# Kernel optimization log

Measured on AMD Instinct MI355X. Metric: run time of the kernel, lower is better.

## Reference

```python
import jax, jax.numpy as jnp
import numpy as np

N_SRC0, N_DST0, N_DST1 = 100000, 25000, 5000
E0, E1 = 800000, 160000
D = 256


def setup_inputs() -> dict:
    key = jax.random.key(0)
    k = jax.random.split(key, 7)
    return {
        "x": jax.random.normal(k[0], (N_SRC0, D), dtype=jnp.float32),
        "ew0": jax.random.uniform(k[1], (E0,), dtype=jnp.float32),
        "ew1": jax.random.uniform(k[2], (E1,), dtype=jnp.float32),
        "src0": jax.random.randint(k[3], (E0,), 0, N_SRC0, dtype=jnp.int32),
        "dst0": jax.random.randint(k[4], (E0,), 0, N_DST0, dtype=jnp.int32),
        "src1": jax.random.randint(k[5], (E1,), 0, N_DST0, dtype=jnp.int32),
        "dst1": jax.random.randint(k[6], (E1,), 0, N_DST1, dtype=jnp.int32),
    }


def _block(x, src, dst, ew, n_dst):
    # u_mul_e + sum: gather src features, scale by edge weight, scatter-sum to dst
    msgs = x[src] * ew[:, None]            # [E, D]
    return jax.ops.segment_sum(msgs, dst, num_segments=n_dst)  # [n_dst, D]


def reference(x, ew0, ew1, src0, dst0, src1, dst1):
    h = _block(x, src0, dst0, ew0, N_DST0)   # block 0: [N_DST0, D]
    h = _block(h, src1, dst1, ew1, N_DST1)   # block 1: [N_DST1, D]
    return h
```

## Files before the change

kernel.cpp:

```cpp
#include <hip/hip_runtime.h>

constexpr int D      = 256;
constexpr int DV4    = D / 4;
constexpr int N_DST0 = 25000;
constexpr int N_DST1 = 5000;
constexpr int CAP    = 96;


__device__ __forceinline__ unsigned pack_bf16(float a, float b) {
    unsigned ua = __float_as_uint(a);
    unsigned ub = __float_as_uint(b);
    ua = (ua + 0x7FFFu + ((ua >> 16) & 1u)) >> 16;
    ub = (ub + 0x7FFFu + ((ub >> 16) & 1u)) >> 16;
    return ua | (ub << 16);
}

__device__ __forceinline__ void fma8_bf16(float* acc, uint4 v, float w) {
    acc[0] += __uint_as_float(v.x << 16)          * w;
    acc[1] += __uint_as_float(v.x & 0xFFFF0000u)  * w;
    acc[2] += __uint_as_float(v.y << 16)          * w;
    acc[3] += __uint_as_float(v.y & 0xFFFF0000u)  * w;
    acc[4] += __uint_as_float(v.z << 16)          * w;
    acc[5] += __uint_as_float(v.z & 0xFFFF0000u)  * w;
    acc[6] += __uint_as_float(v.w << 16)          * w;
    acc[7] += __uint_as_float(v.w & 0xFFFF0000u)  * w;
}


__global__ __launch_bounds__(256) void prep_fused(
    const float4* __restrict__ x4, uint2* __restrict__ xb, int n4,
    const int* __restrict__ src0, const float* __restrict__ ew0,
    const int* __restrict__ dst0, int E0, int* __restrict__ cnt0,
    unsigned long long* __restrict__ meta0,
    const int* __restrict__ src1, const float* __restrict__ ew1,
    const int* __restrict__ dst1, int E1, int* __restrict__ cnt1,
    unsigned long long* __restrict__ meta1)
{
    int third = blockIdx.x / 3;
    int role  = blockIdx.x % 3;
    int nGrp  = gridDim.x / 3;

    if (role < 2) {
        int cb = third * 2 + role;
        int i = cb * blockDim.x + threadIdx.x;
        int stride = nGrp * 2 * blockDim.x;
        for (; i < n4; i += stride) {
            float4 v = x4[i];
            xb[i] = make_uint2(pack_bf16(v.x, v.y), pack_bf16(v.z, v.w));
        }
    } else {
        int T = nGrp * blockDim.x;
        int i0 = third * blockDim.x + threadIdx.x;
        int total = E0 + E1;
        for (int base = i0; base < total; base += 4 * T) {
            int  s[4]; float w[4]; int d[4]; int which[4]; bool ok[4];
            #pragma unroll
            for (int j = 0; j < 4; ++j) {
                int i = base + j * T;
                ok[j] = i < total;
                if (ok[j]) {
                    if (i < E0) { s[j]=src0[i]; w[j]=ew0[i]; d[j]=dst0[i]; which[j]=0; }
                    else { int q=i-E0; s[j]=src1[q]; w[j]=ew1[q]; d[j]=dst1[q]; which[j]=1; }
                }
            }
            int p[4];
            #pragma unroll
            for (int j = 0; j < 4; ++j) {
                if (ok[j]) p[j] = atomicAdd(which[j] ? &cnt1[d[j]] : &cnt0[d[j]], 1);
            }
            #pragma unroll
            for (int j = 0; j < 4; ++j) {
                if (ok[j] && p[j] < CAP) {
                    unsigned long long v =
                        (unsigned long long)(unsigned)s[j] |
                        ((unsigned long long)__float_as_uint(w[j]) << 32);
                    unsigned long long* dstp =
                        (which[j] ? meta1 : meta0) + (size_t)d[j] * CAP + p[j];
                    __builtin_nontemporal_store(v, dstp);
                }
            }
        }
    }
}


template <bool OUT_BF16>
__global__ __launch_bounds__(256) void gather_cap(
    const uint4* __restrict__ xb4,
    const int2*  __restrict__ meta,
    const int*   __restrict__ cnt,
    void*        __restrict__ outp,
    int n_dst)
{
    int wave = (int)((blockIdx.x * blockDim.x + threadIdx.x) >> 6);
    int lane = threadIdx.x & 63;
    if (wave >= n_dst) return;

    int half = lane >> 5;
    int c16  = lane & 31;

    int n = min(cnt[wave], CAP);
    const int2* m = meta + (size_t)wave * CAP;

    float acc[8] = {0.f,0.f,0.f,0.f,0.f,0.f,0.f,0.f};

    for (int base = 0; base < n; base += 64) {
        int idx = base + lane;
        int2 mm = (idx < n) ? m[idx] : make_int2(0, 0);
        int nk = min(64, n - base);

        for (int e = 0; e < nk; e += 8) {
            int   sA = __shfl(mm.x, e + 0 + half, 64);
            int   sB = __shfl(mm.x, e + 2 + half, 64);
            int   sC = __shfl(mm.x, e + 4 + half, 64);
            int   sD = __shfl(mm.x, e + 6 + half, 64);
            float wA = __int_as_float(__shfl(mm.y, e + 0 + half, 64));
            float wB = __int_as_float(__shfl(mm.y, e + 2 + half, 64));
            float wC = __int_as_float(__shfl(mm.y, e + 4 + half, 64));
            float wD = __int_as_float(__shfl(mm.y, e + 6 + half, 64));
            uint4 vA = xb4[(size_t)sA * 32 + c16];
            uint4 vB = xb4[(size_t)sB * 32 + c16];
            uint4 vC = xb4[(size_t)sC * 32 + c16];
            uint4 vD = xb4[(size_t)sD * 32 + c16];
            fma8_bf16(acc, vA, wA);
            fma8_bf16(acc, vB, wB);
            fma8_bf16(acc, vC, wC);
            fma8_bf16(acc, vD, wD);
        }
    }

    #pragma unroll
    for (int j = 0; j < 8; ++j) acc[j] += __shfl_xor(acc[j], 32, 64);

    if (half == 0) {
        if (OUT_BF16) {
            uint4 o;
            o.x = pack_bf16(acc[0], acc[1]);
            o.y = pack_bf16(acc[2], acc[3]);
            o.z = pack_bf16(acc[4], acc[5]);
            o.w = pack_bf16(acc[6], acc[7]);
            ((uint4*)outp)[(size_t)wave * 32 + c16] = o;
        } else {
            float4* o4 = (float4*)outp;
            o4[(size_t)wave * 64 + c16 * 2 + 0] = make_float4(acc[0], acc[1], acc[2], acc[3]);
            o4[(size_t)wave * 64 + c16 * 2 + 1] = make_float4(acc[4], acc[5], acc[6], acc[7]);
        }
    }
}


__global__ __launch_bounds__(256) void hist_both(
    const int* __restrict__ dst0, int E0, int* __restrict__ cnt0,
    const int* __restrict__ dst1, int E1, int* __restrict__ cnt1)
{
    int i = blockIdx.x * blockDim.x + threadIdx.x;
    int stride = gridDim.x * blockDim.x;
    int total = E0 + E1;
    for (; i < total; i += stride) {
        if (i < E0) atomicAdd(&cnt0[dst0[i]], 1);
        else        atomicAdd(&cnt1[dst1[i - E0]], 1);
    }
}

__device__ void scan_one(int* cnt, int* row, int n)
{
    const int T = 1024;
    int t   = threadIdx.x;
    int per = (n + T - 1) / T;
    int b   = t * per;
    int e   = min(b + per, n);

    int local = 0;
    for (int i = b; i < e; ++i) local += cnt[i];

    int lane = t & 63, wid = t >> 6;
    int v = local;
    #pragma unroll
    for (int off = 1; off < 64; off <<= 1) {
        int u = __shfl_up(v, off, 64);
        if (lane >= off) v += u;
    }

    __shared__ int wsum[16], woff[16];
    if (lane == 63) wsum[wid] = v;
    __syncthreads();
    if (t == 0) {
        int run = 0;
        #pragma unroll
        for (int i = 0; i < 16; ++i) { woff[i] = run; run += wsum[i]; }
        row[n] = run;
    }
    __syncthreads();

    int run = woff[wid] + (v - local);
    for (int i = b; i < e; ++i) {
        int c = cnt[i];
        row[i] = run;
        cnt[i] = run;
        run += c;
    }
}

__global__ __launch_bounds__(1024) void scan_both(
    int* cnt0, int* row0, int n0, int* cnt1, int* row1, int n1)
{
    if (blockIdx.x == 0) scan_one(cnt0, row0, n0);
    else                 scan_one(cnt1, row1, n1);
}

__global__ __launch_bounds__(256) void scatter_both(
    const int* __restrict__ src0, const float* __restrict__ ew0,
    const int* __restrict__ dst0, int E0, int* __restrict__ cur0,
    int2* __restrict__ meta0,
    const int* __restrict__ src1, const float* __restrict__ ew1,
    const int* __restrict__ dst1, int E1, int* __restrict__ cur1,
    int2* __restrict__ meta1)
{
    int i = blockIdx.x * blockDim.x + threadIdx.x;
    int stride = gridDim.x * blockDim.x;
    int total = E0 + E1;
    for (; i < total; i += stride) {
        if (i < E0) {
            int p = atomicAdd(&cur0[dst0[i]], 1);
            meta0[p] = make_int2(src0[i], __float_as_int(ew0[i]));
        } else {
            int j = i - E0;
            int p = atomicAdd(&cur1[dst1[j]], 1);
            meta1[p] = make_int2(src1[j], __float_as_int(ew1[j]));
        }
    }
}

__global__ __launch_bounds__(256) void gather_rows_f32(
    const float* __restrict__ xin,
    const int2*  __restrict__ meta,
    const int*   __restrict__ row_start,
    float*       __restrict__ outp,
    int n_dst)
{
    int wave = (int)((blockIdx.x * blockDim.x + threadIdx.x) >> 6);
    int lane = threadIdx.x & 63;
    if (wave >= n_dst) return;

    int beg = row_start[wave];
    int end = row_start[wave + 1];
    const float4* xv = reinterpret_cast<const float4*>(xin);

    float4 acc = {0.f, 0.f, 0.f, 0.f};
    for (int base = beg; base < end; base += 64) {
        int idx = base + lane;
        int2 m = (idx < end) ? meta[idx] : make_int2(0, 0);
        int nk = min(64, end - base);
        int k = 0;
        for (; k + 4 <= nk; k += 4) {
            float4 v0 = xv[(size_t)__shfl(m.x, k + 0, 64) * DV4 + lane];
            float4 v1 = xv[(size_t)__shfl(m.x, k + 1, 64) * DV4 + lane];
            float4 v2 = xv[(size_t)__shfl(m.x, k + 2, 64) * DV4 + lane];
            float4 v3 = xv[(size_t)__shfl(m.x, k + 3, 64) * DV4 + lane];
            float w0 = __int_as_float(__shfl(m.y, k + 0, 64));
            float w1 = __int_as_float(__shfl(m.y, k + 1, 64));
            float w2 = __int_as_float(__shfl(m.y, k + 2, 64));
            float w3 = __int_as_float(__shfl(m.y, k + 3, 64));
            acc.x += v0.x * w0; acc.y += v0.y * w0; acc.z += v0.z * w0; acc.w += v0.w * w0;
            acc.x += v1.x * w1; acc.y += v1.y * w1; acc.z += v1.z * w1; acc.w += v1.w * w1;
            acc.x += v2.x * w2; acc.y += v2.y * w2; acc.z += v2.z * w2; acc.w += v2.w * w2;
            acc.x += v3.x * w3; acc.y += v3.y * w3; acc.z += v3.z * w3; acc.w += v3.w * w3;
        }
        for (; k < nk; ++k) {
            float4 v = xv[(size_t)__shfl(m.x, k, 64) * DV4 + lane];
            float w  = __int_as_float(__shfl(m.y, k, 64));
            acc.x += v.x * w; acc.y += v.y * w; acc.z += v.z * w; acc.w += v.w * w;
        }
    }
    reinterpret_cast<float4*>(outp)[(size_t)wave * DV4 + lane] = acc;
}


extern "C" void kernel_launch(void* const* d_in, const int* in_sizes, int n_in,
                              void* d_out, int out_size, void* d_ws, size_t ws_size,
                              hipStream_t stream) {
    const float* x    = (const float*)d_in[0];
    const float* ew0  = (const float*)d_in[1];
    const float* ew1  = (const float*)d_in[2];
    const int*   src0 = (const int*)d_in[3];
    const int*   dst0 = (const int*)d_in[4];
    const int*   src1 = (const int*)d_in[5];
    const int*   dst1 = (const int*)d_in[6];
    float*       out  = (float*)d_out;

    const int E0    = in_sizes[1];
    const int E1    = in_sizes[2];
    const int N_SRC = in_sizes[0] / D;

    const int blk = 256;
    int g0 = (N_DST0 * 64 + blk - 1) / blk;
    int g1 = (N_DST1 * 64 + blk - 1) / blk;
    int n4 = N_SRC * D / 4;

    size_t need_t1 =
        (size_t)N_SRC * D * 2 +
        (size_t)N_DST0 * D * 2 +
        (size_t)N_DST0 * CAP * 8 +
        (size_t)N_DST1 * CAP * 8 +
        (size_t)(N_DST0 + N_DST1) * 4 + 1024;

    if (ws_size >= need_t1) {
        char* p = (char*)d_ws;
        uint2* xb    = (uint2*)p; p += (size_t)N_SRC * D * 2;
        uint2* h0b   = (uint2*)p; p += (size_t)N_DST0 * D * 2;
        unsigned long long* meta0 = (unsigned long long*)p; p += (size_t)N_DST0 * CAP * 8;
        unsigned long long* meta1 = (unsigned long long*)p; p += (size_t)N_DST1 * CAP * 8;
        int*   cnt0  = (int*)p;   p += (size_t)N_DST0 * 4;
        int*   cnt1  = (int*)p;   p += (size_t)N_DST1 * 4;

        hipMemsetAsync(cnt0, 0, (size_t)(N_DST0 + N_DST1) * 4, stream);

        const int grid = 3072;
        prep_fused<<<grid, blk, 0, stream>>>(
            (const float4*)x, xb, n4,
            src0, ew0, dst0, E0, cnt0, meta0,
            src1, ew1, dst1, E1, cnt1, meta1);

        gather_cap<true ><<<g0, blk, 0, stream>>>(
            (const uint4*)xb,  (const int2*)meta0, cnt0, (void*)h0b, N_DST0);
        gather_cap<false><<<g1, blk, 0, stream>>>(
            (const uint4*)h0b, (const int2*)meta1, cnt1, (void*)out, N_DST1);
    } else {
        char* p = (char*)d_ws;
        float* h0    = (float*)p; p += (size_t)N_DST0 * D * sizeof(float);
        int2*  meta0 = (int2*)p;  p += (size_t)E0 * sizeof(int2);
        int2*  meta1 = (int2*)p;  p += (size_t)E1 * sizeof(int2);
        int*   cnt0  = (int*)p;   p += (size_t)N_DST0 * sizeof(int);
        int*   row0  = (int*)p;   p += (size_t)(N_DST0 + 1) * sizeof(int);
        int*   cnt1  = (int*)p;   p += (size_t)N_DST1 * sizeof(int);
        int*   row1  = (int*)p;   p += (size_t)(N_DST1 + 1) * sizeof(int);

        hipMemsetAsync(cnt0, 0, (size_t)N_DST0 * sizeof(int), stream);
        hipMemsetAsync(cnt1, 0, (size_t)N_DST1 * sizeof(int), stream);

        int gEdges = min((E0 + E1 + blk - 1) / blk, 3840);
        hist_both<<<gEdges, blk, 0, stream>>>(dst0, E0, cnt0, dst1, E1, cnt1);
        scan_both<<<2, 1024, 0, stream>>>(cnt0, row0, N_DST0, cnt1, row1, N_DST1);
        scatter_both<<<gEdges, blk, 0, stream>>>(src0, ew0, dst0, E0, cnt0, meta0,
                                                 src1, ew1, dst1, E1, cnt1, meta1);
        gather_rows_f32<<<g0, blk, 0, stream>>>(x,  meta0, row0, h0,  N_DST0);
        gather_rows_f32<<<g1, blk, 0, stream>>>(h0, meta1, row1, out, N_DST1);
    }
}
```

Measured before the change: 146.7 us.

## Pad per-destination atomic counters to separate cache lines and rebalance prep blocks

Counters are now spaced 16 ints (64 bytes) apart so each destination's atomic counter sits on its own line, which is meant to reduce same-line contention. Block roles change from interleaved thirds to contiguous ranges: 1024 blocks convert x to bf16 and 2048 blocks scatter edges, so more blocks now handle edges. The 4-way unrolled edge loop with nontemporal stores becomes a simple grid-stride loop with plain stores. The cost is a 16x larger counter memset and scattered counter reads in the gather kernels.

```diff
diff --git a/kernel.cpp b/kernel.cpp
--- a/kernel.cpp
+++ b/kernel.cpp
@@ -1,10 +1,11 @@
 #include <hip/hip_runtime.h>
 
-constexpr int D      = 256;
-constexpr int DV4    = D / 4;
-constexpr int N_DST0 = 25000;
-constexpr int N_DST1 = 5000;
-constexpr int CAP    = 96;
+constexpr int D       = 256;
+constexpr int DV4     = D / 4;
+constexpr int N_DST0  = 25000;
+constexpr int N_DST1  = 5000;
+constexpr int CAP     = 96;
+constexpr int CSTRIDE = 16;
 
 
 __device__ __forceinline__ unsigned pack_bf16(float a, float b) {
@@ -28,7 +29,7 @@
 
 
 __global__ __launch_bounds__(256) void prep_fused(
-    const float4* __restrict__ x4, uint2* __restrict__ xb, int n4,
+    const float4* __restrict__ x4, uint2* __restrict__ xb, int n4, int Gc,
     const int* __restrict__ src0, const float* __restrict__ ew0,
     const int* __restrict__ dst0, int E0, int* __restrict__ cnt0,
     unsigned long long* __restrict__ meta0,
@@ -36,48 +37,37 @@
     const int* __restrict__ dst1, int E1, int* __restrict__ cnt1,
     unsigned long long* __restrict__ meta1)
 {
-    int third = blockIdx.x / 3;
-    int role  = blockIdx.x % 3;
-    int nGrp  = gridDim.x / 3;
-
-    if (role < 2) {
-        int cb = third * 2 + role;
-        int i = cb * blockDim.x + threadIdx.x;
-        int stride = nGrp * 2 * blockDim.x;
+    if (blockIdx.x < Gc) {
+        int i = blockIdx.x * blockDim.x + threadIdx.x;
+        int stride = Gc * blockDim.x;
         for (; i < n4; i += stride) {
             float4 v = x4[i];
             xb[i] = make_uint2(pack_bf16(v.x, v.y), pack_bf16(v.z, v.w));
         }
     } else {
-        int T = nGrp * blockDim.x;
-        int i0 = third * blockDim.x + threadIdx.x;
+        int i = (blockIdx.x - Gc) * blockDim.x + threadIdx.x;
+        int stride = (gridDim.x - Gc) * blockDim.x;
         int total = E0 + E1;
-        for (int base = i0; base < total; base += 4 * T) {
-            int  s[4]; float w[4]; int d[4]; int which[4]; bool ok[4];
-            #pragma unroll
-            for (int j = 0; j < 4; ++j) {
-                int i = base + j * T;
-                ok[j] = i < total;
-                if (ok[j]) {
-                    if (i < E0) { s[j]=src0[i]; w[j]=ew0[i]; d[j]=dst0[i]; which[j]=0; }
-                    else { int q=i-E0; s[j]=src1[q]; w[j]=ew1[q]; d[j]=dst1[q]; which[j]=1; }
-                }
-            }
-            int p[4];
-            #pragma unroll
-            for (int j = 0; j < 4; ++j) {
-                if (ok[j]) p[j] = atomicAdd(which[j] ? &cnt1[d[j]] : &cnt0[d[j]], 1);
-            }
-            #pragma unroll
-            for (int j = 0; j < 4; ++j) {
-                if (ok[j] && p[j] < CAP) {
-                    unsigned long long v =
-                        (unsigned long long)(unsigned)s[j] |
-                        ((unsigned long long)__float_as_uint(w[j]) << 32);
-                    unsigned long long* dstp =
-                        (which[j] ? meta1 : meta0) + (size_t)d[j] * CAP + p[j];
-                    __builtin_nontemporal_store(v, dstp);
-                }
+        for (; i < total; i += stride) {
+            if (i < E0) {
+                int s = src0[i];
+                float w = ew0[i];
+                int d = dst0[i];
+                int p = atomicAdd(&cnt0[(size_t)d * CSTRIDE], 1);
+                if (p < CAP)
+                    meta0[(size_t)d * CAP + p] =
+                        (unsigned long long)(unsigned)s |
+                        ((unsigned long long)__float_as_uint(w) << 32);
+            } else {
+                int q = i - E0;
+                int s = src1[q];
+                float w = ew1[q];
+                int d = dst1[q];
+                int p = atomicAdd(&cnt1[(size_t)d * CSTRIDE], 1);
+                if (p < CAP)
+                    meta1[(size_t)d * CAP + p] =
+                        (unsigned long long)(unsigned)s |
+                        ((unsigned long long)__float_as_uint(w) << 32);
             }
         }
     }
@@ -99,7 +89,7 @@
     int half = lane >> 5;
     int c16  = lane & 31;
 
-    int n = min(cnt[wave], CAP);
+    int n = min(cnt[(size_t)wave * CSTRIDE], CAP);
     const int2* m = meta + (size_t)wave * CAP;
 
     float acc[8] = {0.f,0.f,0.f,0.f,0.f,0.f,0.f,0.f};
@@ -302,7 +292,8 @@
         (size_t)N_DST0 * D * 2 +
         (size_t)N_DST0 * CAP * 8 +
         (size_t)N_DST1 * CAP * 8 +
-        (size_t)(N_DST0 + N_DST1) * 4 + 1024;
+        (size_t)(N_DST0 + N_DST1) * CSTRIDE * 4 +
+        1024;
 
     if (ws_size >= need_t1) {
         char* p = (char*)d_ws;
@@ -310,14 +301,14 @@
         uint2* h0b   = (uint2*)p; p += (size_t)N_DST0 * D * 2;
         unsigned long long* meta0 = (unsigned long long*)p; p += (size_t)N_DST0 * CAP * 8;
         unsigned long long* meta1 = (unsigned long long*)p; p += (size_t)N_DST1 * CAP * 8;
-        int*   cnt0  = (int*)p;   p += (size_t)N_DST0 * 4;
-        int*   cnt1  = (int*)p;   p += (size_t)N_DST1 * 4;
-
-        hipMemsetAsync(cnt0, 0, (size_t)(N_DST0 + N_DST1) * 4, stream);
-
-        const int grid = 3072;
-        prep_fused<<<grid, blk, 0, stream>>>(
-            (const float4*)x, xb, n4,
+        int*   cnt0  = (int*)p;   p += (size_t)N_DST0 * CSTRIDE * 4;
+        int*   cnt1  = (int*)p;   p += (size_t)N_DST1 * CSTRIDE * 4;
+
+        hipMemsetAsync(cnt0, 0, (size_t)(N_DST0 + N_DST1) * CSTRIDE * 4, stream);
+
+        const int Gc = 1024, Gs = 2048;
+        prep_fused<<<Gc + Gs, blk, 0, stream>>>(
+            (const float4*)x, xb, n4, Gc,
             src0, ew0, dst0, E0, cnt0, meta0,
             src1, ew1, dst1, E1, cnt1, meta1);
 
```

Measured after the change: 139.9 us. 4.6% less time.
